# Optimization experiments

Hardware: AMD Instinct MI355X
Metric: run time of the kernel (lower is better)

The kernel has to match this reference:

```python
import jax, jax.numpy as jnp
from jax import lax
import numpy as np

D_MODEL, D_STATE, D_CONV, EXPAND = 1024, 16, 4, 2
D_INNER = EXPAND * D_MODEL          # 2048
DT_RANK = D_MODEL // 16             # 64
B_SZ, L_SEQ = 2, 2048


def setup_inputs() -> dict:
    key = jax.random.key(0)
    ks = jax.random.split(key, 8)
    x = jax.random.normal(ks[0], (B_SZ, L_SEQ, D_MODEL), jnp.float32)
    inp = {
        "x": x,
        "ln_g": jnp.ones((D_MODEL,), jnp.float32),
        "ln_b": jnp.zeros((D_MODEL,), jnp.float32),
        # fan-in scaled weights for numerical sanity
        "W_in": jax.random.normal(ks[1], (2 * D_INNER, D_MODEL), jnp.float32) / np.sqrt(D_MODEL),
        "conv_w": jax.random.normal(ks[2], (D_INNER, D_CONV), jnp.float32) / np.sqrt(D_CONV),
        "conv_b": jnp.zeros((D_INNER,), jnp.float32),
        "W_xp": jax.random.normal(ks[3], (DT_RANK + 2 * D_STATE, D_INNER), jnp.float32) / np.sqrt(D_INNER),
        "W_dt": jax.random.normal(ks[4], (D_INNER, DT_RANK), jnp.float32) / np.sqrt(DT_RANK),
        "b_dt": jax.random.normal(ks[5], (D_INNER,), jnp.float32) * 0.1 - 4.0,  # softplus(dt) small, like mamba init
        # S4D-real init: A = -exp(A_log), A_log = log(1..d_state)
        "A_log": jnp.broadcast_to(jnp.log(jnp.arange(1, D_STATE + 1, dtype=jnp.float32)), (D_INNER, D_STATE)).copy(),
        "D": jnp.ones((D_INNER,), jnp.float32),
        "W_out": jax.random.normal(ks[6], (D_MODEL, D_INNER), jnp.float32) / np.sqrt(D_INNER),
    }
    return inp


def _selective_scan(u, dt, A, Bm, Cm, Dvec):
    # u, dt: (B, L, d_inner); Bm, Cm: (B, L, d_state); A: (d_inner, d_state)
    def step(h, inputs):
        u_t, dt_t, B_t, C_t = inputs                      # (B,di),(B,di),(B,n),(B,n)
        dA = jnp.exp(dt_t[:, :, None] * A[None])          # (B,di,n), in (0,1) since A<0
        dBu = (dt_t * u_t)[:, :, None] * B_t[:, None, :]  # (B,di,n)
        h = dA * h + dBu
        y = jnp.einsum('bdn,bn->bd', h, C_t)
        return h, y
    xs = (u.transpose(1, 0, 2), dt.transpose(1, 0, 2),
          Bm.transpose(1, 0, 2), Cm.transpose(1, 0, 2))
    h0 = jnp.zeros((u.shape[0], u.shape[2], A.shape[1]), u.dtype)
    _, ys = lax.scan(step, h0, xs)
    return ys.transpose(1, 0, 2) + u * Dvec               # (B, L, d_inner)


def reference(x, ln_g, ln_b, W_in, conv_w, conv_b, W_xp, W_dt, b_dt, A_log, D, W_out):
    d_inner, d_conv = conv_w.shape
    dt_rank = W_dt.shape[1]
    d_state = A_log.shape[1]
    # pre-LayerNorm
    mu = jnp.mean(x, axis=-1, keepdims=True)
    var = jnp.mean(jnp.square(x - mu), axis=-1, keepdims=True)
    xn = (x - mu) * lax.rsqrt(var + 1e-5) * ln_g + ln_b
    # input projection -> (B, L, 2*d_inner)
    xz = jnp.einsum('bld,ed->ble', xn, W_in)
    u, z = jnp.split(xz, 2, axis=-1)
    # causal depthwise conv over time
    u_c = lax.conv_general_dilated(
        u.transpose(0, 2, 1),                 # (B, d_inner, L)
        conv_w[:, None, :],                   # (d_inner, 1, d_conv)
        window_strides=(1,), padding=[(d_conv - 1, 0)],
        feature_group_count=d_inner)
    u_c = jax.nn.silu((u_c + conv_b[None, :, None]).transpose(0, 2, 1))  # (B, L, d_inner)
    # data-dependent dt, B, C
    x_dbl = jnp.einsum('bld,ed->ble', u_c, W_xp)
    dt, Bm, Cm = jnp.split(x_dbl, [dt_rank, dt_rank + d_state], axis=-1)
    dt = jax.nn.softplus(jnp.einsum('blr,dr->bld', dt, W_dt) + b_dt)
    A = -jnp.exp(A_log)
    y = _selective_scan(u_c, dt, A, Bm, Cm, D)
    y = y * jax.nn.silu(z)
    out = jnp.einsum('ble,de->bld', y, W_out)
    return x + out
```

## Files before the change

### kernel.cpp

```cpp
#include <hip/hip_runtime.h>

typedef __bf16 bf16x8 __attribute__((ext_vector_type(8)));
typedef float  f32x4  __attribute__((ext_vector_type(4)));

#define LOG2E 1.44269504088896f

__device__ __forceinline__ float bfl(unsigned short s) {
    return __uint_as_float(((unsigned int)s) << 16);
}
__device__ __forceinline__ unsigned short f2bf(float f) {
    unsigned int x = __float_as_uint(f);
    x += 0x7fffu + ((x >> 16) & 1u);
    return (unsigned short)(x >> 16);
}
__device__ __forceinline__ float fexp2(float x) { return __builtin_amdgcn_exp2f(x); }
__device__ __forceinline__ float fexp(float x)  { return __builtin_amdgcn_exp2f(x * LOG2E); }
__device__ __forceinline__ float frcp(float x)  { return __builtin_amdgcn_rcpf(x); }
__device__ __forceinline__ float silu_f(float x) {
    return x * frcp(1.f + fexp2(-x * LOG2E));
}
__device__ __forceinline__ void gl_lds(const unsigned short* g, unsigned short* l) {
    __builtin_amdgcn_global_load_lds(
        (__attribute__((address_space(1))) const void*)g,
        (__attribute__((address_space(3))) void*)l, 16, 0, 0);
}

#define BSZ   2
#define LSEQ  2048
#define DMODEL 1024
#define DI    2048
#define DS    16
#define NCH   64
#define CL    32

#define WI_N   4194304
#define WXP_N  196608
#define WDT_N  131072
#define WOUT_N 2097152
#define WSEG1  (WI_N)
#define WSEG2  (WI_N + WXP_N)
#define WSEG3  (WI_N + WXP_N + WDT_N)
#define WTOT   (WI_N + WXP_N + WDT_N + WOUT_N)

__global__ __launch_bounds__(256) void cvt_weights(
    const float* __restrict__ w0, const float* __restrict__ w1,
    const float* __restrict__ w2, const float* __restrict__ w3,
    unsigned short* __restrict__ dst)
{
    const size_t e0 = ((size_t)blockIdx.x * 256 + threadIdx.x) * 8;
    if (e0 >= WTOT) return;
    const float* src;
    size_t off;
    if      (e0 < WSEG1) { src = w0; off = e0; }
    else if (e0 < WSEG2) { src = w1; off = e0 - WSEG1; }
    else if (e0 < WSEG3) { src = w2; off = e0 - WSEG2; }
    else                 { src = w3; off = e0 - WSEG3; }
    float4 a = *(const float4*)(src + off);
    float4 b = *(const float4*)(src + off + 4);
    ushort4 lo, hi;
    lo.x = f2bf(a.x); lo.y = f2bf(a.y); lo.z = f2bf(a.z); lo.w = f2bf(a.w);
    hi.x = f2bf(b.x); hi.y = f2bf(b.y); hi.z = f2bf(b.z); hi.w = f2bf(b.w);
    *(ushort4*)(dst + e0) = lo;
    *(ushort4*)(dst + e0 + 4) = hi;
}

__global__ __launch_bounds__(256) void ln_kernel(
    const float* __restrict__ x,
    const float* __restrict__ g,
    const float* __restrict__ b,
    unsigned short* __restrict__ xn)
{
    const int row = blockIdx.x;
    const int tid = threadIdx.x;
    const int lane = tid & 63, wv = tid >> 6;
    const float* xp = x + (size_t)row * DMODEL;

    float4 v = ((const float4*)xp)[tid];
    float s = v.x + v.y + v.z + v.w;
    float q = v.x*v.x + v.y*v.y + v.z*v.z + v.w*v.w;
    #pragma unroll
    for (int o = 32; o > 0; o >>= 1) {
        s += __shfl_down(s, o);
        q += __shfl_down(q, o);
    }
    __shared__ float ss[4], sq[4];
    if (lane == 0) { ss[wv] = s; sq[wv] = q; }
    __syncthreads();
    s = ss[0] + ss[1] + ss[2] + ss[3];
    q = sq[0] + sq[1] + sq[2] + sq[3];
    const float mu  = s * (1.f / DMODEL);
    const float var = q * (1.f / DMODEL) - mu * mu;
    const float rs  = rsqrtf(var + 1e-5f);

    float4 gv = ((const float4*)g)[tid];
    float4 bv = ((const float4*)b)[tid];
    ushort4 o;
    o.x = f2bf((v.x - mu) * rs * gv.x + bv.x);
    o.y = f2bf((v.y - mu) * rs * gv.y + bv.y);
    o.z = f2bf((v.z - mu) * rs * gv.z + bv.z);
    o.w = f2bf((v.w - mu) * rs * gv.w + bv.w);
    ((ushort4*)(xn + (size_t)row * DMODEL))[tid] = o;
}

template<int EPI, int LOGM>
__global__ __launch_bounds__(512, 2) void gemm_pipe(
    const unsigned short* __restrict__ A,
    const unsigned short* __restrict__ Bw,
    void* __restrict__ Cout,
    const void* __restrict__ aux0,
    int K, int ldc)
{
    __shared__ unsigned short As[2][256 * 64];
    __shared__ unsigned short Bs[2][128 * 64];
    const int tid  = threadIdx.x;
    const int lane = tid & 63;
    const int wid  = tid >> 6;
    const int wm   = (wid >> 2) * 128;
    const int wn   = (wid & 3) * 32;

    const int nwg = gridDim.x;
    const int id  = blockIdx.x;
    const int swz = (id & 7) * (nwg >> 3) + (id >> 3);
    const int bx  = swz & ((1 << LOGM) - 1);
    const int by  = swz >> LOGM;
    const size_t am0 = (size_t)bx * 256;
    const size_t bn0 = (size_t)by * 128;

    const int srow  = lane >> 3;
    const int sslot = (lane & 7) ^ srow;
    const unsigned short* gA = A  + (am0 + wid * 32 + srow) * (size_t)K + sslot * 8;
    const unsigned short* gB = Bw + (bn0 + wid * 16 + srow) * (size_t)K + sslot * 8;
    unsigned short* lA0 = &As[0][(wid * 32) * 64];
    unsigned short* lB0 = &Bs[0][(wid * 16) * 64];
    unsigned short* lA1 = &As[1][(wid * 32) * 64];
    unsigned short* lB1 = &Bs[1][(wid * 16) * 64];

    const int NT = K >> 6;
    #pragma unroll
    for (int j = 0; j < 4; ++j) gl_lds(gA + (size_t)(8 * j) * K,       lA0 + j * 512);
    #pragma unroll
    for (int j = 0; j < 2; ++j) gl_lds(gB + (size_t)(8 * j) * K,       lB0 + j * 512);
    #pragma unroll
    for (int j = 0; j < 4; ++j) gl_lds(gA + (size_t)(8 * j) * K + 64,  lA1 + j * 512);
    #pragma unroll
    for (int j = 0; j < 2; ++j) gl_lds(gB + (size_t)(8 * j) * K + 64,  lB1 + j * 512);

    f32x4 acc[8][2];
    f32x4 z4 = {0.f, 0.f, 0.f, 0.f};
    #pragma unroll
    for (int i = 0; i < 8; ++i) { acc[i][0] = z4; acc[i][1] = z4; }

    const int lr  = lane & 15;
    const int lq  = lane >> 4;
    const int key = lr & 7;

    for (int t = 0; t < NT; ++t) {
        const int cur = t & 1;
        if (t < NT - 1) asm volatile("s_waitcnt vmcnt(6)" ::: "memory");
        else            asm volatile("s_waitcnt vmcnt(0)" ::: "memory");
        __builtin_amdgcn_s_barrier();
        __builtin_amdgcn_sched_barrier(0);

        bf16x8 af[8][2], bfv[2][2];
        #pragma unroll
        for (int fm = 0; fm < 8; ++fm)
            #pragma unroll
            for (int ks = 0; ks < 2; ++ks)
                af[fm][ks] = *(const bf16x8*)
                    &As[cur][(wm + fm * 16 + lr) * 64 + ((ks * 4 + lq) ^ key) * 8];
        #pragma unroll
        for (int fn = 0; fn < 2; ++fn)
            #pragma unroll
            for (int ks = 0; ks < 2; ++ks)
                bfv[fn][ks] = *(const bf16x8*)
                    &Bs[cur][(wn + fn * 16 + lr) * 64 + ((ks * 4 + lq) ^ key) * 8];
        asm volatile("s_waitcnt lgkmcnt(0)" ::: "memory");
        __builtin_amdgcn_sched_barrier(0);
        __builtin_amdgcn_s_barrier();

        if (t + 2 < NT) {
            const size_t ko = (size_t)(t + 2) * 64;
            unsigned short* dA = (cur ? lA1 : lA0);
            unsigned short* dB = (cur ? lB1 : lB0);
            #pragma unroll
            for (int j = 0; j < 4; ++j) gl_lds(gA + (size_t)(8 * j) * K + ko, dA + j * 512);
            #pragma unroll
            for (int j = 0; j < 2; ++j) gl_lds(gB + (size_t)(8 * j) * K + ko, dB + j * 512);
        }

        __builtin_amdgcn_s_setprio(1);
        #pragma unroll
        for (int fm = 0; fm < 8; ++fm)
            #pragma unroll
            for (int fn = 0; fn < 2; ++fn) {
                acc[fm][fn] = __builtin_amdgcn_mfma_f32_16x16x32_bf16(
                    af[fm][0], bfv[fn][0], acc[fm][fn], 0, 0, 0);
                acc[fm][fn] = __builtin_amdgcn_mfma_f32_16x16x32_bf16(
                    af[fm][1], bfv[fn][1], acc[fm][fn], 0, 0, 0);
            }
        __builtin_amdgcn_s_setprio(0);
    }

    const int er = lq * 4;
    const int ec = lr;
    #pragma unroll
    for (int fm = 0; fm < 8; ++fm) {
        #pragma unroll
        for (int fn = 0; fn < 2; ++fn) {
            const size_t col = bn0 + wn + fn * 16 + ec;
            #pragma unroll
            for (int r = 0; r < 4; ++r) {
                const size_t row = am0 + wm + fm * 16 + er + r;
                float v = acc[fm][fn][r];
                if constexpr (EPI == 0) {
                    ((unsigned short*)Cout)[row * ldc + col] = f2bf(v);
                } else {
                    float t2 = v + ((const float*)aux0)[row * ldc + col];
                    ((float*)Cout)[row * ldc + col] = t2;
                }
            }
        }
    }
}

template<int BM, int BN, int EPI, int LOG_NBXM>
__global__ __launch_bounds__(256) void gemm_lds(
    const unsigned short* __restrict__ A,
    const unsigned short* __restrict__ Bw,
    void* __restrict__ Cout,
    const void* __restrict__ aux0,
    int K, int ldc)
{
    constexpr int FM = BM / 32;
    constexpr int FN = BN / 32;
    __shared__ unsigned short As[BM * 64];
    __shared__ unsigned short Bs[BN * 64];
    const int tid  = threadIdx.x;
    const int lane = tid & 63;
    const int wv   = tid >> 6;
    const int wm   = (wv >> 1) * (BM / 2);
    const int wn   = (wv & 1)  * (BN / 2);

    const int nwg = gridDim.x;
    const int id  = blockIdx.x;
    const int swz = (id & 7) * (nwg >> 3) + (id >> 3);
    const int bx  = swz & ((1 << LOG_NBXM) - 1);
    const int by  = swz >> LOG_NBXM;

    f32x4 acc[FM][FN];
    f32x4 z4 = {0.f, 0.f, 0.f, 0.f};
    #pragma unroll
    for (int i = 0; i < FM; ++i)
        #pragma unroll
        for (int j = 0; j < FN; ++j) acc[i][j] = z4;

    const size_t am0 = (size_t)bx * BM;
    const size_t bn0 = (size_t)by * BN;
    const int srow  = lane >> 3;
    const int scol  = (lane & 7) * 8;

    for (int k0 = 0; k0 < K; k0 += 64) {
        __syncthreads();
        #pragma unroll
        for (int i = 0; i < BM / 32; ++i) {
            const int rb = (wv * (BM / 32) + i) * 8;
            gl_lds(&A[(am0 + rb + srow) * (size_t)K + k0 + scol], &As[rb * 64]);
        }
        #pragma unroll
        for (int i = 0; i < BN / 32; ++i) {
            const int rb = (wv * (BN / 32) + i) * 8;
            gl_lds(&Bw[(bn0 + rb + srow) * (size_t)K + k0 + scol], &Bs[rb * 64]);
        }
        __syncthreads();
        const int lr = lane & 15, lk = (lane >> 4) * 8;
        #pragma unroll
        for (int ks = 0; ks < 2; ++ks) {
            bf16x8 af[FM], bfv[FN];
            #pragma unroll
            for (int fm = 0; fm < FM; ++fm)
                af[fm] = *(const bf16x8*)&As[(wm + fm * 16 + lr) * 64 + ks * 32 + lk];
            #pragma unroll
            for (int fn = 0; fn < FN; ++fn)
                bfv[fn] = *(const bf16x8*)&Bs[(wn + fn * 16 + lr) * 64 + ks * 32 + lk];
            #pragma unroll
            for (int fm = 0; fm < FM; ++fm)
                #pragma unroll
                for (int fn = 0; fn < FN; ++fn)
                    acc[fm][fn] = __builtin_amdgcn_mfma_f32_16x16x32_bf16(
                        af[fm], bfv[fn], acc[fm][fn], 0, 0, 0);
        }
    }

    const int er = (lane >> 4) * 4;
    const int ec = lane & 15;
    #pragma unroll
    for (int fm = 0; fm < FM; ++fm) {
        #pragma unroll
        for (int fn = 0; fn < FN; ++fn) {
            const size_t col = bn0 + wn + fn * 16 + ec;
            #pragma unroll
            for (int r = 0; r < 4; ++r) {
                const size_t row = am0 + wm + fm * 16 + er + r;
                float v = acc[fm][fn][r];
                if constexpr (EPI == 0) {
                    ((unsigned short*)Cout)[row * ldc + col] = f2bf(v);
                } else if constexpr (EPI == 2) {
                    float t = v + ((const float*)aux0)[col];
                    float e = fexp2(t * LOG2E);
                    float sp = 0.69314718056f * __builtin_amdgcn_logf(1.f + e);
                    if (t > 20.f) sp = t;
                    ((unsigned short*)Cout)[row * ldc + col] = f2bf(sp);
                } else {
                    float t = v + ((const float*)aux0)[row * ldc + col];
                    ((float*)Cout)[row * ldc + col] = t;
                }
            }
        }
    }
}

__global__ __launch_bounds__(256) void gemm4_splitk(
    const unsigned short* __restrict__ A,
    const unsigned short* __restrict__ Bw,
    float* __restrict__ Cpart)
{
    constexpr int LDP = 72;
    __shared__ unsigned short As[64 * LDP];
    __shared__ unsigned short Bs[96 * LDP];
    const int tid  = threadIdx.x;
    const int lane = tid & 63;
    const int wv   = tid >> 6;
    const int wm   = (wv >> 1) * 32;
    const int wn   = (wv & 1)  * 48;

    f32x4 acc[2][3];
    f32x4 z4 = {0.f, 0.f, 0.f, 0.f};
    #pragma unroll
    for (int i = 0; i < 2; ++i)
        #pragma unroll
        for (int j = 0; j < 3; ++j) acc[i][j] = z4;

    const size_t am0 = (size_t)blockIdx.x * 64;
    const int kz = blockIdx.y;
    const int kbeg = kz * 256;
    const int r0 = tid >> 3;
    const int c0 = (tid & 7) * 8;

    for (int k0 = kbeg; k0 < kbeg + 256; k0 += 64) {
        __syncthreads();
        #pragma unroll
        for (int p = 0; p < 2; ++p) {
            int r = r0 + p * 32;
            *(uint4*)&As[r * LDP + c0] = *(const uint4*)&A[(am0 + r) * (size_t)2048 + k0 + c0];
        }
        #pragma unroll
        for (int p = 0; p < 3; ++p) {
            int r = r0 + p * 32;
            *(uint4*)&Bs[r * LDP + c0] = *(const uint4*)&Bw[(size_t)r * 2048 + k0 + c0];
        }
        __syncthreads();
        const int lr = lane & 15, lk = (lane >> 4) * 8;
        #pragma unroll
        for (int ks = 0; ks < 2; ++ks) {
            bf16x8 af[2], bfv[3];
            #pragma unroll
            for (int fm = 0; fm < 2; ++fm)
                af[fm] = *(const bf16x8*)&As[(wm + fm * 16 + lr) * LDP + ks * 32 + lk];
            #pragma unroll
            for (int fn = 0; fn < 3; ++fn)
                bfv[fn] = *(const bf16x8*)&Bs[(wn + fn * 16 + lr) * LDP + ks * 32 + lk];
            #pragma unroll
            for (int fm = 0; fm < 2; ++fm)
                #pragma unroll
                for (int fn = 0; fn < 3; ++fn)
                    acc[fm][fn] = __builtin_amdgcn_mfma_f32_16x16x32_bf16(
                        af[fm], bfv[fn], acc[fm][fn], 0, 0, 0);
        }
    }

    const int er = (lane >> 4) * 4;
    const int ec = lane & 15;
    float* out = Cpart + (size_t)kz * 4096 * 96;
    #pragma unroll
    for (int fm = 0; fm < 2; ++fm) {
        #pragma unroll
        for (int fn = 0; fn < 3; ++fn) {
            const int col = wn + fn * 16 + ec;
            #pragma unroll
            for (int r = 0; r < 4; ++r) {
                const size_t row = am0 + wm + fm * 16 + er + r;
                out[row * 96 + col] = acc[fm][fn][r];
            }
        }
    }
}

__global__ __launch_bounds__(256) void reduce_xdbl(
    const float* __restrict__ Cpart,
    float* __restrict__ x_dbl,
    unsigned short* __restrict__ dtlow)
{
    const int e = blockIdx.x * 256 + threadIdx.x;
    float s = 0.f;
    #pragma unroll
    for (int kz = 0; kz < 8; ++kz) s += Cpart[(size_t)kz * 393216 + e];
    x_dbl[e] = s;
    const int row = e / 96, col = e - row * 96;
    if (col < 64) dtlow[row * 64 + col] = f2bf(s);
}

__global__ __launch_bounds__(256) void conv_silu(
    const unsigned short* __restrict__ xz,
    const float* __restrict__ convw,
    const float* __restrict__ convb,
    unsigned short* __restrict__ u_c)
{
    const size_t i = (size_t)blockIdx.x * 256 + threadIdx.x;
    if (i >= (size_t)BSZ * LSEQ * DI) return;
    const int d = (int)(i & (DI - 1));
    const size_t bl = i >> 11;
    const int l = (int)(bl & (LSEQ - 1));
    const int b = (int)(bl >> 11);

    float4 wv = *(const float4*)&convw[d * 4];
    float acc = convb[d];
    const size_t rowbase = (size_t)(b * LSEQ) * (2 * DI) + d;
    if (l >= 3) acc += bfl(xz[rowbase + (size_t)(l - 3) * (2 * DI)]) * wv.x;
    if (l >= 2) acc += bfl(xz[rowbase + (size_t)(l - 2) * (2 * DI)]) * wv.y;
    if (l >= 1) acc += bfl(xz[rowbase + (size_t)(l - 1) * (2 * DI)]) * wv.z;
    acc += bfl(xz[rowbase + (size_t)l * (2 * DI)]) * wv.w;
    u_c[i] = f2bf(silu_f(acc));
}

__device__ __forceinline__ bool load_A(const float* __restrict__ A_log, int d, float* An2) {
    bool fast = true;
    #pragma unroll
    for (int i = 0; i < 4; ++i) {
        float4 a = *(const float4*)&A_log[(size_t)d * DS + i * 4];
        float e0 = fexp(a.x), e1 = fexp(a.y), e2 = fexp(a.z), e3 = fexp(a.w);
        fast = fast && fabsf(e0 - (4*i+1)) < 1e-3f * (4*i+1)
                    && fabsf(e1 - (4*i+2)) < 1e-3f * (4*i+2)
                    && fabsf(e2 - (4*i+3)) < 1e-3f * (4*i+3)
                    && fabsf(e3 - (4*i+4)) < 1e-3f * (4*i+4);
        An2[4*i+0] = -e0 * LOG2E; An2[4*i+1] = -e1 * LOG2E;
        An2[4*i+2] = -e2 * LOG2E; An2[4*i+3] = -e3 * LOG2E;
    }
    return fast;
}

__global__ __launch_bounds__(256) void scan1(
    const unsigned short* __restrict__ dt,
    const unsigned short* __restrict__ u_c,
    const float* __restrict__ x_dbl,
    const float* __restrict__ A_log,
    float* __restrict__ chunk_h,
    float* __restrict__ Ssum)
{
    const int d = blockIdx.x * 256 + threadIdx.x;
    const int b = blockIdx.y, c = blockIdx.z;
    const int tid = threadIdx.x;

    __shared__ float sB[CL][DS];
    if (tid < 128) {
        int s = tid >> 2, j = (tid & 3) * 4;
        *(float4*)&sB[s][j] =
            *(const float4*)&x_dbl[(size_t)(b * LSEQ + c * CL + s) * 96 + 64 + j];
    }

    float An2[DS];
    const bool fast = load_A(A_log, d, An2);
    __syncthreads();

    float h[DS];
    #pragma unroll
    for (int n = 0; n < DS; ++n) h[n] = 0.f;
    float S = 0.f;
    const size_t base = (size_t)(b * LSEQ + c * CL) * DI + d;
    if (fast) {
        for (int s = 0; s < CL; ++s) {
            float dtt = bfl(dt[base + (size_t)s * DI]);
            float ut  = bfl(u_c[base + (size_t)s * DI]);
            S += dtt;
            float dtu = dtt * ut;
            float e1 = fexp2(-dtt * LOG2E);
            float p = 1.f;
            #pragma unroll
            for (int n = 0; n < DS; ++n) {
                p *= e1;
                h[n] = p * h[n] + dtu * sB[s][n];
            }
        }
    } else {
        for (int s = 0; s < CL; ++s) {
            float dtt = bfl(dt[base + (size_t)s * DI]);
            float ut  = bfl(u_c[base + (size_t)s * DI]);
            S += dtt;
            float dtu = dtt * ut;
            #pragma unroll
            for (int n = 0; n < DS; ++n) {
                float dA = fexp2(dtt * An2[n]);
                h[n] = dA * h[n] + dtu * sB[s][n];
            }
        }
    }
    const size_t co = ((size_t)((b * NCH + c) * DI) + d) * DS;
    #pragma unroll
    for (int n = 0; n < DS; ++n) chunk_h[co + n] = h[n];
    Ssum[(size_t)(b * NCH + c) * DI + d] = S;
}

__global__ __launch_bounds__(256) void scan2(
    float* __restrict__ chunk_h,
    const float* __restrict__ Ssum,
    const float* __restrict__ A_log)
{
    const int gid = blockIdx.x * 256 + threadIdx.x;
    const int b = gid >> 15;
    const int rem = gid & 32767;
    const int d = rem >> 4;
    const int n = rem & 15;
    const float A2 = -fexp(A_log[(size_t)d * DS + n]) * LOG2E;
    float H = 0.f;
    for (int c = 0; c < NCH; ++c) {
        const size_t idx = ((size_t)((b * NCH + c) * DI) + d) * DS + n;
        float hl = chunk_h[idx];
        float S  = Ssum[(size_t)(b * NCH + c) * DI + d];
        chunk_h[idx] = H;
        H = fexp2(A2 * S) * H + hl;
    }
}

__global__ __launch_bounds__(256) void scan3(
    const unsigned short* __restrict__ dt,
    const unsigned short* __restrict__ u_c,
    const float* __restrict__ x_dbl,
    const float* __restrict__ A_log,
    const float* __restrict__ Hstart,
    const float* __restrict__ Dvec,
    const unsigned short* __restrict__ xz,
    unsigned short* __restrict__ yb)
{
    const int d = blockIdx.x * 256 + threadIdx.x;
    const int b = blockIdx.y, c = blockIdx.z;
    const int tid = threadIdx.x;

    __shared__ float sBC[CL][32];
    {
        int s = tid >> 3, j = (tid & 7) * 4;
        *(float4*)&sBC[s][j] =
            *(const float4*)&x_dbl[(size_t)(b * LSEQ + c * CL + s) * 96 + 64 + j];
    }

    float An2[DS];
    const bool fast = load_A(A_log, d, An2);
    const float Dd = Dvec[d];
    float h[DS];
    const size_t co = ((size_t)((b * NCH + c) * DI) + d) * DS;
    #pragma unroll
    for (int n = 0; n < DS; ++n) h[n] = Hstart[co + n];
    __syncthreads();

    const size_t base  = (size_t)(b * LSEQ + c * CL) * DI + d;
    const size_t zbase = (size_t)(b * LSEQ + c * CL) * (2 * DI) + DI + d;
    if (fast) {
        for (int s = 0; s < CL; ++s) {
            float dtt = bfl(dt[base + (size_t)s * DI]);
            float ut  = bfl(u_c[base + (size_t)s * DI]);
            float dtu = dtt * ut;
            float e1 = fexp2(-dtt * LOG2E);
            float p = 1.f;
            float a0 = 0.f, a1 = 0.f;
            #pragma unroll
            for (int n = 0; n < DS; ++n) {
                p *= e1;
                h[n] = p * h[n] + dtu * sBC[s][n];
                if (n & 1) a1 += h[n] * sBC[s][16 + n];
                else       a0 += h[n] * sBC[s][16 + n];
            }
            float y = a0 + a1 + Dd * ut;
            float z = bfl(xz[zbase + (size_t)s * (2 * DI)]);
            yb[base + (size_t)s * DI] = f2bf(y * silu_f(z));
        }
    } else {
        for (int s = 0; s < CL; ++s) {
            float dtt = bfl(dt[base + (size_t)s * DI]);
            float ut  = bfl(u_c[base + (size_t)s * DI]);
            float dtu = dtt * ut;
            float a0 = 0.f, a1 = 0.f;
            #pragma unroll
            for (int n = 0; n < DS; ++n) {
                float dA = fexp2(dtt * An2[n]);
                h[n] = dA * h[n] + dtu * sBC[s][n];
                if (n & 1) a1 += h[n] * sBC[s][16 + n];
                else       a0 += h[n] * sBC[s][16 + n];
            }
            float y = a0 + a1 + Dd * ut;
            float z = bfl(xz[zbase + (size_t)s * (2 * DI)]);
            yb[base + (size_t)s * DI] = f2bf(y * silu_f(z));
        }
    }
}

extern "C" void kernel_launch(void* const* d_in, const int* in_sizes, int n_in,
                              void* d_out, int out_size, void* d_ws, size_t ws_size,
                              hipStream_t stream) {
    const float* x      = (const float*)d_in[0];
    const float* ln_g   = (const float*)d_in[1];
    const float* ln_b   = (const float*)d_in[2];
    const float* W_in   = (const float*)d_in[3];
    const float* conv_w = (const float*)d_in[4];
    const float* conv_b = (const float*)d_in[5];
    const float* W_xp   = (const float*)d_in[6];
    const float* W_dt   = (const float*)d_in[7];
    const float* b_dt   = (const float*)d_in[8];
    const float* A_log  = (const float*)d_in[9];
    const float* Dv     = (const float*)d_in[10];
    const float* W_out  = (const float*)d_in[11];
    float* out = (float*)d_out;

    char* w = (char*)d_ws;
    unsigned short* xn     = (unsigned short*)(w + 0);
    unsigned short* xz     = (unsigned short*)(w + 8388608);
    unsigned short* u_c    = (unsigned short*)(w + 41943040);
    float*          x_dbl  = (float*)         (w + 58720256);
    unsigned short* dtlow  = (unsigned short*)(w + 60293120);
    unsigned short* dtb    = (unsigned short*)(w + 60817408);
    float*          chunkh = (float*)         (w + 77594624);
    float*          Ssum   = (float*)         (w + 94371840);
    unsigned short* yb     = (unsigned short*)(w + 95420416);
    unsigned short* wbf    = (unsigned short*)(w + 112197632);
    float*          Cpart  = (float*)         (w + 125435904);
    unsigned short* Wi_bf   = wbf;
    unsigned short* Wxp_bf  = wbf + WSEG1;
    unsigned short* Wdt_bf  = wbf + WSEG2;
    unsigned short* Wout_bf = wbf + WSEG3;
    (void)in_sizes; (void)n_in; (void)out_size; (void)ws_size;

    const int MROWS = BSZ * LSEQ;

    cvt_weights<<<(WTOT / 8 + 255) / 256, 256, 0, stream>>>(
        W_in, W_xp, W_dt, W_out, wbf);
    ln_kernel<<<MROWS, 256, 0, stream>>>(x, ln_g, ln_b, xn);
    gemm_pipe<0, 4><<<512, 512, 0, stream>>>(
        xn, Wi_bf, xz, nullptr, DMODEL, 2 * DI);
    conv_silu<<<(MROWS * DI) / 256, 256, 0, stream>>>(xz, conv_w, conv_b, u_c);
    gemm4_splitk<<<dim3(64, 8), 256, 0, stream>>>(u_c, Wxp_bf, Cpart);
    reduce_xdbl<<<(MROWS * 96) / 256, 256, 0, stream>>>(Cpart, x_dbl, dtlow);
    gemm_lds<128, 64, 2, 5><<<1024, 256, 0, stream>>>(
        dtlow, Wdt_bf, dtb, b_dt, 64, DI);
    scan1<<<dim3(DI / 256, BSZ, NCH), 256, 0, stream>>>(
        dtb, u_c, x_dbl, A_log, chunkh, Ssum);
    scan2<<<(BSZ * DI * DS) / 256, 256, 0, stream>>>(chunkh, Ssum, A_log);
    scan3<<<dim3(DI / 256, BSZ, NCH), 256, 0, stream>>>(
        dtb, u_c, x_dbl, A_log, chunkh, Dv, xz, yb);
    gemm_lds<128, 64, 3, 5><<<512, 256, 0, stream>>>(
        yb, Wout_bf, out, x, DI, DMODEL);
}
```

Baseline: 206.1 us.

## Fuse LN with weight cast, retile GEMMs to 128x128, vectorize conv

Merges the layer-norm and weight-conversion kernels into a single launch to save one launch. Replaces the 256x128 pipelined GEMM with a 128x128 variant that splits the A-fragment reads into two halves, so LDS reads overlap with MFMA work. The in-projection now runs on 1024 blocks and the out-projection moves from gemm_lds to the new kernel. The depthwise conv is vectorized to 8 channels per thread with 16-byte loads. Smaller tiles give more blocks but less data reuse per tile.

```diff
diff --git a/kernel.cpp b/kernel.cpp
--- a/kernel.cpp
+++ b/kernel.cpp
@@ -2,6 +2,7 @@
 
 typedef __bf16 bf16x8 __attribute__((ext_vector_type(8)));
 typedef float  f32x4  __attribute__((ext_vector_type(4)));
+typedef unsigned short u16x8 __attribute__((ext_vector_type(8)));
 
 #define LOG2E 1.44269504088896f
 
@@ -41,170 +42,177 @@
 #define WSEG2  (WI_N + WXP_N)
 #define WSEG3  (WI_N + WXP_N + WDT_N)
 #define WTOT   (WI_N + WXP_N + WDT_N + WOUT_N)
-
-__global__ __launch_bounds__(256) void cvt_weights(
+#define CVT_BLOCKS 3232
+
+__global__ __launch_bounds__(256) void ln_cvt(
+    const float* __restrict__ x,
+    const float* __restrict__ g,
+    const float* __restrict__ b,
+    unsigned short* __restrict__ xn,
     const float* __restrict__ w0, const float* __restrict__ w1,
     const float* __restrict__ w2, const float* __restrict__ w3,
     unsigned short* __restrict__ dst)
 {
-    const size_t e0 = ((size_t)blockIdx.x * 256 + threadIdx.x) * 8;
-    if (e0 >= WTOT) return;
-    const float* src;
-    size_t off;
-    if      (e0 < WSEG1) { src = w0; off = e0; }
-    else if (e0 < WSEG2) { src = w1; off = e0 - WSEG1; }
-    else if (e0 < WSEG3) { src = w2; off = e0 - WSEG2; }
-    else                 { src = w3; off = e0 - WSEG3; }
-    float4 a = *(const float4*)(src + off);
-    float4 b = *(const float4*)(src + off + 4);
-    ushort4 lo, hi;
-    lo.x = f2bf(a.x); lo.y = f2bf(a.y); lo.z = f2bf(a.z); lo.w = f2bf(a.w);
-    hi.x = f2bf(b.x); hi.y = f2bf(b.y); hi.z = f2bf(b.z); hi.w = f2bf(b.w);
-    *(ushort4*)(dst + e0) = lo;
-    *(ushort4*)(dst + e0 + 4) = hi;
-}
-
-__global__ __launch_bounds__(256) void ln_kernel(
-    const float* __restrict__ x,
-    const float* __restrict__ g,
-    const float* __restrict__ b,
-    unsigned short* __restrict__ xn)
-{
-    const int row = blockIdx.x;
     const int tid = threadIdx.x;
-    const int lane = tid & 63, wv = tid >> 6;
-    const float* xp = x + (size_t)row * DMODEL;
-
-    float4 v = ((const float4*)xp)[tid];
-    float s = v.x + v.y + v.z + v.w;
-    float q = v.x*v.x + v.y*v.y + v.z*v.z + v.w*v.w;
-    #pragma unroll
-    for (int o = 32; o > 0; o >>= 1) {
-        s += __shfl_down(s, o);
-        q += __shfl_down(q, o);
-    }
-    __shared__ float ss[4], sq[4];
-    if (lane == 0) { ss[wv] = s; sq[wv] = q; }
-    __syncthreads();
-    s = ss[0] + ss[1] + ss[2] + ss[3];
-    q = sq[0] + sq[1] + sq[2] + sq[3];
-    const float mu  = s * (1.f / DMODEL);
-    const float var = q * (1.f / DMODEL) - mu * mu;
-    const float rs  = rsqrtf(var + 1e-5f);
-
-    float4 gv = ((const float4*)g)[tid];
-    float4 bv = ((const float4*)b)[tid];
-    ushort4 o;
-    o.x = f2bf((v.x - mu) * rs * gv.x + bv.x);
-    o.y = f2bf((v.y - mu) * rs * gv.y + bv.y);
-    o.z = f2bf((v.z - mu) * rs * gv.z + bv.z);
-    o.w = f2bf((v.w - mu) * rs * gv.w + bv.w);
-    ((ushort4*)(xn + (size_t)row * DMODEL))[tid] = o;
-}
-
-template<int EPI, int LOGM>
-__global__ __launch_bounds__(512, 2) void gemm_pipe(
+    if (blockIdx.x < BSZ * LSEQ) {
+        const int row = blockIdx.x;
+        const int lane = tid & 63, wv = tid >> 6;
+        const float* xp = x + (size_t)row * DMODEL;
+
+        float4 v = ((const float4*)xp)[tid];
+        float s = v.x + v.y + v.z + v.w;
+        float q = v.x*v.x + v.y*v.y + v.z*v.z + v.w*v.w;
+        #pragma unroll
+        for (int o = 32; o > 0; o >>= 1) {
+            s += __shfl_down(s, o);
+            q += __shfl_down(q, o);
+        }
+        __shared__ float ss[4], sq[4];
+        if (lane == 0) { ss[wv] = s; sq[wv] = q; }
+        __syncthreads();
+        s = ss[0] + ss[1] + ss[2] + ss[3];
+        q = sq[0] + sq[1] + sq[2] + sq[3];
+        const float mu  = s * (1.f / DMODEL);
+        const float var = q * (1.f / DMODEL) - mu * mu;
+        const float rs  = rsqrtf(var + 1e-5f);
+
+        float4 gv = ((const float4*)g)[tid];
+        float4 bv = ((const float4*)b)[tid];
+        ushort4 o;
+        o.x = f2bf((v.x - mu) * rs * gv.x + bv.x);
+        o.y = f2bf((v.y - mu) * rs * gv.y + bv.y);
+        o.z = f2bf((v.z - mu) * rs * gv.z + bv.z);
+        o.w = f2bf((v.w - mu) * rs * gv.w + bv.w);
+        ((ushort4*)(xn + (size_t)row * DMODEL))[tid] = o;
+    } else {
+        const size_t e0 = ((size_t)(blockIdx.x - BSZ * LSEQ) * 256 + tid) * 8;
+        if (e0 >= WTOT) return;
+        const float* src;
+        size_t off;
+        if      (e0 < WSEG1) { src = w0; off = e0; }
+        else if (e0 < WSEG2) { src = w1; off = e0 - WSEG1; }
+        else if (e0 < WSEG3) { src = w2; off = e0 - WSEG2; }
+        else                 { src = w3; off = e0 - WSEG3; }
+        float4 a = *(const float4*)(src + off);
+        float4 bb = *(const float4*)(src + off + 4);
+        ushort4 lo, hi;
+        lo.x = f2bf(a.x);  lo.y = f2bf(a.y);  lo.z = f2bf(a.z);  lo.w = f2bf(a.w);
+        hi.x = f2bf(bb.x); hi.y = f2bf(bb.y); hi.z = f2bf(bb.z); hi.w = f2bf(bb.w);
+        *(ushort4*)(dst + e0) = lo;
+        *(ushort4*)(dst + e0 + 4) = hi;
+    }
+}
+
+template<int EPI, int LOGNB>
+__global__ __launch_bounds__(512, 2) void gemm_pipe128(
     const unsigned short* __restrict__ A,
     const unsigned short* __restrict__ Bw,
     void* __restrict__ Cout,
     const void* __restrict__ aux0,
     int K, int ldc)
 {
-    __shared__ unsigned short As[2][256 * 64];
+    __shared__ unsigned short As[2][128 * 64];
     __shared__ unsigned short Bs[2][128 * 64];
     const int tid  = threadIdx.x;
     const int lane = tid & 63;
     const int wid  = tid >> 6;
-    const int wm   = (wid >> 2) * 128;
+    const int wm   = (wid >> 2) * 64;
     const int wn   = (wid & 3) * 32;
 
     const int nwg = gridDim.x;
     const int id  = blockIdx.x;
     const int swz = (id & 7) * (nwg >> 3) + (id >> 3);
-    const int bx  = swz & ((1 << LOGM) - 1);
-    const int by  = swz >> LOGM;
-    const size_t am0 = (size_t)bx * 256;
-    const size_t bn0 = (size_t)by * 128;
+    const int bn_i = swz & ((1 << LOGNB) - 1);
+    const int bm_i = swz >> LOGNB;
+    const size_t am0 = (size_t)bm_i * 128;
+    const size_t bn0 = (size_t)bn_i * 128;
 
     const int srow  = lane >> 3;
     const int sslot = (lane & 7) ^ srow;
-    const unsigned short* gA = A  + (am0 + wid * 32 + srow) * (size_t)K + sslot * 8;
+    const unsigned short* gA = A  + (am0 + wid * 16 + srow) * (size_t)K + sslot * 8;
     const unsigned short* gB = Bw + (bn0 + wid * 16 + srow) * (size_t)K + sslot * 8;
-    unsigned short* lA0 = &As[0][(wid * 32) * 64];
-    unsigned short* lB0 = &Bs[0][(wid * 16) * 64];
-    unsigned short* lA1 = &As[1][(wid * 32) * 64];
-    unsigned short* lB1 = &Bs[1][(wid * 16) * 64];
 
     const int NT = K >> 6;
-    #pragma unroll
-    for (int j = 0; j < 4; ++j) gl_lds(gA + (size_t)(8 * j) * K,       lA0 + j * 512);
-    #pragma unroll
-    for (int j = 0; j < 2; ++j) gl_lds(gB + (size_t)(8 * j) * K,       lB0 + j * 512);
-    #pragma unroll
-    for (int j = 0; j < 4; ++j) gl_lds(gA + (size_t)(8 * j) * K + 64,  lA1 + j * 512);
-    #pragma unroll
-    for (int j = 0; j < 2; ++j) gl_lds(gB + (size_t)(8 * j) * K + 64,  lB1 + j * 512);
-
-    f32x4 acc[8][2];
+
+#define STAGE128(buf, ko)                                                      \
+    {   _Pragma("unroll")                                                      \
+        for (int j = 0; j < 2; ++j)                                            \
+            gl_lds(gA + (size_t)(j * 8) * K + (ko), &As[buf][(wid * 16 + j * 8) * 64]); \
+        _Pragma("unroll")                                                      \
+        for (int j = 0; j < 2; ++j)                                            \
+            gl_lds(gB + (size_t)(j * 8) * K + (ko), &Bs[buf][(wid * 16 + j * 8) * 64]); }
+
+    STAGE128(0, 0)
+    STAGE128(1, 64)
+
+    f32x4 acc[4][2];
     f32x4 z4 = {0.f, 0.f, 0.f, 0.f};
     #pragma unroll
-    for (int i = 0; i < 8; ++i) { acc[i][0] = z4; acc[i][1] = z4; }
+    for (int i = 0; i < 4; ++i) { acc[i][0] = z4; acc[i][1] = z4; }
 
     const int lr  = lane & 15;
     const int lq  = lane >> 4;
     const int key = lr & 7;
 
+#define RD_A128(dst, h)                                                        \
+    _Pragma("unroll")                                                          \
+    for (int i = 0; i < 2; ++i)                                                \
+        _Pragma("unroll")                                                      \
+        for (int ks = 0; ks < 2; ++ks)                                         \
+            dst[i][ks] = *(const bf16x8*)&As[cur][(wm + ((h) * 2 + i) * 16 + lr) * 64 \
+                                                  + (((ks * 4 + lq) ^ key) * 8)];
+
+#define MFMA_H(src, h)                                                         \
+    _Pragma("unroll")                                                          \
+    for (int i = 0; i < 2; ++i)                                                \
+        _Pragma("unroll")                                                      \
+        for (int fn = 0; fn < 2; ++fn) {                                       \
+            acc[(h) * 2 + i][fn] = __builtin_amdgcn_mfma_f32_16x16x32_bf16(    \
+                src[i][0], bfv[fn][0], acc[(h) * 2 + i][fn], 0, 0, 0);         \
+            acc[(h) * 2 + i][fn] = __builtin_amdgcn_mfma_f32_16x16x32_bf16(    \
+                src[i][1], bfv[fn][1], acc[(h) * 2 + i][fn], 0, 0, 0);         }
+
     for (int t = 0; t < NT; ++t) {
         const int cur = t & 1;
-        if (t < NT - 1) asm volatile("s_waitcnt vmcnt(6)" ::: "memory");
+        if (t < NT - 1) asm volatile("s_waitcnt vmcnt(4)" ::: "memory");
         else            asm volatile("s_waitcnt vmcnt(0)" ::: "memory");
         __builtin_amdgcn_s_barrier();
         __builtin_amdgcn_sched_barrier(0);
 
-        bf16x8 af[8][2], bfv[2][2];
-        #pragma unroll
-        for (int fm = 0; fm < 8; ++fm)
+        bf16x8 bfv[2][2], fA[2][2], fB[2][2];
+        #pragma unroll
+        for (int fn = 0; fn < 2; ++fn)
             #pragma unroll
             for (int ks = 0; ks < 2; ++ks)
-                af[fm][ks] = *(const bf16x8*)
-                    &As[cur][(wm + fm * 16 + lr) * 64 + ((ks * 4 + lq) ^ key) * 8];
-        #pragma unroll
-        for (int fn = 0; fn < 2; ++fn)
-            #pragma unroll
-            for (int ks = 0; ks < 2; ++ks)
-                bfv[fn][ks] = *(const bf16x8*)
-                    &Bs[cur][(wn + fn * 16 + lr) * 64 + ((ks * 4 + lq) ^ key) * 8];
+                bfv[fn][ks] = *(const bf16x8*)&Bs[cur][(wn + fn * 16 + lr) * 64
+                                                        + (((ks * 4 + lq) ^ key) * 8)];
+        RD_A128(fA, 0)
         asm volatile("s_waitcnt lgkmcnt(0)" ::: "memory");
         __builtin_amdgcn_sched_barrier(0);
+
+        RD_A128(fB, 1)
+        __builtin_amdgcn_s_setprio(1);
+        MFMA_H(fA, 0)
+        __builtin_amdgcn_s_setprio(0);
+        asm volatile("s_waitcnt lgkmcnt(0)" ::: "memory");
+        __builtin_amdgcn_sched_barrier(0);
+
         __builtin_amdgcn_s_barrier();
-
         if (t + 2 < NT) {
-            const size_t ko = (size_t)(t + 2) * 64;
-            unsigned short* dA = (cur ? lA1 : lA0);
-            unsigned short* dB = (cur ? lB1 : lB0);
-            #pragma unroll
-            for (int j = 0; j < 4; ++j) gl_lds(gA + (size_t)(8 * j) * K + ko, dA + j * 512);
-            #pragma unroll
-            for (int j = 0; j < 2; ++j) gl_lds(gB + (size_t)(8 * j) * K + ko, dB + j * 512);
-        }
-
+            STAGE128(cur, (size_t)(t + 2) * 64)
+        }
         __builtin_amdgcn_s_setprio(1);
-        #pragma unroll
-        for (int fm = 0; fm < 8; ++fm)
-            #pragma unroll
-            for (int fn = 0; fn < 2; ++fn) {
-                acc[fm][fn] = __builtin_amdgcn_mfma_f32_16x16x32_bf16(
-                    af[fm][0], bfv[fn][0], acc[fm][fn], 0, 0, 0);
-                acc[fm][fn] = __builtin_amdgcn_mfma_f32_16x16x32_bf16(
-                    af[fm][1], bfv[fn][1], acc[fm][fn], 0, 0, 0);
-            }
+        MFMA_H(fB, 1)
         __builtin_amdgcn_s_setprio(0);
     }
+#undef RD_A128
+#undef MFMA_H
+#undef STAGE128
 
     const int er = lq * 4;
     const int ec = lr;
     #pragma unroll
-    for (int fm = 0; fm < 8; ++fm) {
+    for (int fm = 0; fm < 4; ++fm) {
         #pragma unroll
         for (int fn = 0; fn < 2; ++fn) {
             const size_t col = bn0 + wn + fn * 16 + ec;
@@ -409,27 +417,46 @@
     if (col < 64) dtlow[row * 64 + col] = f2bf(s);
 }
 
-__global__ __launch_bounds__(256) void conv_silu(
+__global__ __launch_bounds__(256) void conv_silu8(
     const unsigned short* __restrict__ xz,
     const float* __restrict__ convw,
     const float* __restrict__ convb,
     unsigned short* __restrict__ u_c)
 {
-    const size_t i = (size_t)blockIdx.x * 256 + threadIdx.x;
-    if (i >= (size_t)BSZ * LSEQ * DI) return;
-    const int d = (int)(i & (DI - 1));
-    const size_t bl = i >> 11;
-    const int l = (int)(bl & (LSEQ - 1));
-    const int b = (int)(bl >> 11);
-
-    float4 wv = *(const float4*)&convw[d * 4];
-    float acc = convb[d];
-    const size_t rowbase = (size_t)(b * LSEQ) * (2 * DI) + d;
-    if (l >= 3) acc += bfl(xz[rowbase + (size_t)(l - 3) * (2 * DI)]) * wv.x;
-    if (l >= 2) acc += bfl(xz[rowbase + (size_t)(l - 2) * (2 * DI)]) * wv.y;
-    if (l >= 1) acc += bfl(xz[rowbase + (size_t)(l - 1) * (2 * DI)]) * wv.z;
-    acc += bfl(xz[rowbase + (size_t)l * (2 * DI)]) * wv.w;
-    u_c[i] = f2bf(silu_f(acc));
+    const int i = blockIdx.x * 256 + threadIdx.x;
+    const int dg = i & (DI / 8 - 1);
+    const int bl = i >> 8;
+    const int l = bl & (LSEQ - 1);
+    const int b = bl >> 11;
+    const int d0 = dg * 8;
+
+    float4 wv[8];
+    #pragma unroll
+    for (int j = 0; j < 8; ++j) wv[j] = *(const float4*)&convw[(d0 + j) * 4];
+    float acc[8];
+    {
+        float4 cb0 = *(const float4*)&convb[d0];
+        float4 cb1 = *(const float4*)&convb[d0 + 4];
+        acc[0] = cb0.x; acc[1] = cb0.y; acc[2] = cb0.z; acc[3] = cb0.w;
+        acc[4] = cb1.x; acc[5] = cb1.y; acc[6] = cb1.z; acc[7] = cb1.w;
+    }
+    const size_t rowbase = (size_t)(b * LSEQ) * (2 * DI) + d0;
+    #pragma unroll
+    for (int k = 0; k < 4; ++k) {
+        const int lr = l - 3 + k;
+        if (lr >= 0) {
+            u16x8 v = *(const u16x8*)&xz[rowbase + (size_t)lr * (2 * DI)];
+            #pragma unroll
+            for (int j = 0; j < 8; ++j) {
+                float w = (k == 0) ? wv[j].x : (k == 1) ? wv[j].y : (k == 2) ? wv[j].z : wv[j].w;
+                acc[j] += bfl(v[j]) * w;
+            }
+        }
+    }
+    u16x8 o;
+    #pragma unroll
+    for (int j = 0; j < 8; ++j) o[j] = f2bf(silu_f(acc[j]));
+    *(u16x8*)&u_c[(size_t)bl * DI + d0] = o;
 }
 
 __device__ __forceinline__ bool load_A(const float* __restrict__ A_log, int d, float* An2) {
@@ -638,12 +665,11 @@
 
     const int MROWS = BSZ * LSEQ;
 
-    cvt_weights<<<(WTOT / 8 + 255) / 256, 256, 0, stream>>>(
-        W_in, W_xp, W_dt, W_out, wbf);
-    ln_kernel<<<MROWS, 256, 0, stream>>>(x, ln_g, ln_b, xn);
-    gemm_pipe<0, 4><<<512, 512, 0, stream>>>(
+    ln_cvt<<<MROWS + CVT_BLOCKS, 256, 0, stream>>>(
+        x, ln_g, ln_b, xn, W_in, W_xp, W_dt, W_out, wbf);
+    gemm_pipe128<0, 5><<<1024, 512, 0, stream>>>(
         xn, Wi_bf, xz, nullptr, DMODEL, 2 * DI);
-    conv_silu<<<(MROWS * DI) / 256, 256, 0, stream>>>(xz, conv_w, conv_b, u_c);
+    conv_silu8<<<(MROWS * DI / 8) / 256, 256, 0, stream>>>(xz, conv_w, conv_b, u_c);
     gemm4_splitk<<<dim3(64, 8), 256, 0, stream>>>(u_c, Wxp_bf, Cpart);
     reduce_xdbl<<<(MROWS * 96) / 256, 256, 0, stream>>>(Cpart, x_dbl, dtlow);
     gemm_lds<128, 64, 2, 5><<<1024, 256, 0, stream>>>(
@@ -653,6 +679,6 @@
     scan2<<<(BSZ * DI * DS) / 256, 256, 0, stream>>>(chunkh, Ssum, A_log);
     scan3<<<dim3(DI / 256, BSZ, NCH), 256, 0, stream>>>(
         dtb, u_c, x_dbl, A_log, chunkh, Dv, xz, yb);
-    gemm_lds<128, 64, 3, 5><<<512, 256, 0, stream>>>(
+    gemm_pipe128<3, 3><<<256, 512, 0, stream>>>(
         yb, Wout_bf, out, x, DI, DMODEL);
 }
```

Result: faster. 191.6 us (-7.0%).
